# Kernel optimization log

Measured on AMD Instinct MI355X. Metric: run time of the kernel, lower is better.

Reference implementation:

```python
import jax, jax.numpy as jnp
import numpy as np

ORDER = 2
BN_EPS = 1e-5

def setup_inputs() -> dict:
    key = jax.random.key(0)
    ks = jax.random.split(key, 8)
    B, N, L, H = 32, 512, 12, 64
    S = 2                      # support_len
    OUT = 64                   # out_dim
    M = ORDER * S * H          # einsum middle dim = 256
    x = jax.random.normal(ks[0], (B, N, L, H), dtype=jnp.float32)
    # row-scaled random diffusion matrices to keep multi-hop propagation stable
    support = jax.random.uniform(ks[1], (S, N, N), dtype=jnp.float32) / N
    scale = 1.0 / M
    weight = scale * jax.random.normal(ks[2], (L, M, OUT), dtype=jnp.float32)
    eps = jnp.zeros((1,), dtype=jnp.float32)
    gamma = jnp.ones((OUT,), dtype=jnp.float32)
    beta = jnp.zeros((OUT,), dtype=jnp.float32)
    w2 = jax.random.normal(ks[3], (OUT, OUT), dtype=jnp.float32) / np.sqrt(OUT)
    b2 = jnp.zeros((OUT,), dtype=jnp.float32)
    return {"x": x, "support": support, "weight": weight, "eps": eps,
            "gamma": gamma, "beta": beta, "w2": w2, "b2": b2}

def reference(x, support, weight, eps, gamma, beta, w2, b2):
    B, N, L, H = x.shape
    xv = x.reshape(B, N, L * H)            # [B,N,LH]
    res = []
    for i in range(support.shape[0]):      # small fixed loop over supports
        A = support[i]                     # [N,N]
        out = xv
        for _ in range(ORDER):
            out = (1.0 + eps) * out + jnp.einsum('nm,bmd->bnd', A, out)
            res.append(out)
    out = jnp.stack(res, axis=-1)          # [B,N,LH,K], K = order*support_len
    K = out.shape[-1]
    out = out.reshape(B, N, L, H * K)      # [B,N,L,M]
    out = jnp.einsum('bnlm,lmo->bno', out, weight)   # [B,N,OUT]
    # dropout is identity in eval mode
    C = out.shape[-1]
    flat = out.reshape(B * N, C)
    mean = flat.mean(axis=0)
    var = flat.var(axis=0)                 # biased, matching torch BN training
    normed = (flat - mean) * jax.lax.rsqrt(var + BN_EPS) * gamma + beta
    y = jax.nn.relu(normed.reshape(B, N, C))
    return jnp.einsum('bnc,oc->bno', y, w2) + b2
```

## Files before the change

kernel.cpp:

```cpp
#include <hip/hip_runtime.h>
#include <hip/hip_bf16.h>
#include <cstddef>
#include <cstdint>

#define B_   32
#define N_   512
#define D_   768
#define OUT_ 64
#define R_   (B_ * N_)

typedef unsigned short u16;
typedef __bf16 bf16x8 __attribute__((ext_vector_type(8)));
typedef float  f32x4  __attribute__((ext_vector_type(4)));
typedef unsigned short u16x8 __attribute__((ext_vector_type(8)));

__device__ __forceinline__ u16 f2bf(float f) {
    __hip_bfloat16 h = __float2bfloat16(f);
    return __builtin_bit_cast(u16, h);
}

__device__ __forceinline__ f32x4 mfma16(u16x8 a, u16x8 b, f32x4 c) {
    return __builtin_amdgcn_mfma_f32_16x16x32_bf16(
        __builtin_bit_cast(bf16x8, a), __builtin_bit_cast(bf16x8, b), c, 0, 0, 0);
}

__device__ __forceinline__ void gl2lds16(const void* g, void* l) {
    __builtin_amdgcn_global_load_lds(
        (const __attribute__((address_space(1))) unsigned int*)g,
        (__attribute__((address_space(3))) unsigned int*)l, 16, 0, 0);
}

__global__ __launch_bounds__(256) void prep2(
    const float* __restrict__ support, const float* __restrict__ weight,
    const float* __restrict__ epsp,
    u16* __restrict__ MallC, u16* __restrict__ MT, u16* __restrict__ Wt)
{
    const int blk = blockIdx.x, tid = threadIdx.x;
    __shared__ float t[32][33];
    if (blk < 512) {
        int s = blk >> 8, rem = blk & 255;
        int n0 = (rem >> 4) * 32, m0 = (rem & 15) * 32;
        const float f = 1.0f + epsp[0];
        const float* S = support + (size_t)s * 262144;
#pragma unroll
        for (int p = 0; p < 4; ++p) {
            int nl = p * 8 + (tid >> 5), ml = tid & 31;
            float v = S[(size_t)(n0 + nl) * 512 + m0 + ml];
            if (n0 + nl == m0 + ml) v += f;
            MallC[(size_t)(n0 + nl) * 2048 + s * 1024 + m0 + ml] = f2bf(v);
            t[nl][ml] = v;
        }
        __syncthreads();
#pragma unroll
        for (int p = 0; p < 4; ++p) {
            int ml = p * 8 + (tid >> 5), nl = tid & 31;
            MT[(size_t)s * 262144 + (size_t)(m0 + ml) * 512 + n0 + nl] = f2bf(t[nl][ml]);
        }
    } else {
        int idx = (blk - 512) * 256 + tid;
        int k = idx / 49152, rem = idx % 49152;
        int o = rem / 768, d = rem % 768;
        int l = d >> 6, hh = d & 63;
        Wt[idx] = f2bf(weight[((size_t)l * 256 + hh * 4 + k) * 64 + o]);
    }
}

__global__ __launch_bounds__(256) void zgemm_fused(
    const u16* __restrict__ Wt, const float* __restrict__ x,
    const u16* __restrict__ MallC_in, const u16* __restrict__ MT,
    u16* __restrict__ Z, u16* __restrict__ MallC_out)
{
    __shared__ __align__(16) char smem[32768];
    const int tid = threadIdx.x, lane = tid & 63, wid = tid >> 6;
    const int wr = wid >> 1, wc = wid & 1;
    const int lrow = lane & 15, lk = (lane >> 4) * 8;
    const int q = lane >> 4;
    const int bid = blockIdx.x;

    if (bid < 512) {
        u16* As = (u16*)smem;
        u16* Bs = (u16*)(smem + 16384);
        const int rt = bid >> 1, y = bid & 1;
        const int j0 = rt * 64;

        const u16* gsrcA[4]; u16* ldstA[4];
#pragma unroll
        for (int t = 0; t < 4; ++t) {
            int idx = wid * 4 + t;
            int pan = idx >> 3, sub = idx & 7;
            gsrcA[t] = Wt + (size_t)(y * 128 + sub * 16 + lrow) * 768 + pan * 32 + lk;
            ldstA[t] = As + pan * 4096 + sub * 512;
        }
        const int brow = tid & 63, kp = tid >> 6;
        const f32x4* gx = (const f32x4*)(x + (size_t)(j0 + brow) * 768 + kp * 16);
        u16* bdst = Bs + (kp >> 1) * 2048 + (brow >> 4) * 512 + (brow & 15) * 8;
        const int bo0 = (kp & 1) * 2 * 128, bo1 = bo0 + 128;

        f32x4 acc[4][2] = {};
        for (int kk = 0; kk < 12; ++kk) {
#pragma unroll
            for (int t = 0; t < 4; ++t) gl2lds16(gsrcA[t], ldstA[t]);
#pragma unroll
            for (int t = 0; t < 4; ++t) gsrcA[t] += 64;
            f32x4 a0 = gx[0], a1 = gx[1], a2 = gx[2], a3 = gx[3];
            gx += 16;
            u16x8 w0, w1;
#pragma unroll
            for (int j = 0; j < 4; ++j) {
                w0[j] = f2bf(a0[j]); w0[4 + j] = f2bf(a1[j]);
                w1[j] = f2bf(a2[j]); w1[4 + j] = f2bf(a3[j]);
            }
            *(u16x8*)(bdst + bo0) = w0;
            *(u16x8*)(bdst + bo1) = w1;
            __syncthreads();
#pragma unroll
            for (int pan = 0; pan < 2; ++pan) {
                u16x8 af[4], bq[2];
#pragma unroll
                for (int f = 0; f < 4; ++f)
                    af[f] = *(const u16x8*)(As + pan * 4096 + (wr * 4 + f) * 512 + lane * 8);
#pragma unroll
                for (int f = 0; f < 2; ++f)
                    bq[f] = *(const u16x8*)(Bs + pan * 2048 + (wc * 2 + f) * 512 + lane * 8);
#pragma unroll
                for (int fi = 0; fi < 4; ++fi)
#pragma unroll
                    for (int fj = 0; fj < 2; ++fj)
                        acc[fi][fj] = mfma16(af[fi], bq[fj], acc[fi][fj]);
            }
            __syncthreads();
        }
        u16* Rw = (u16*)smem + wid * 2560;
#pragma unroll
        for (int fi = 0; fi < 4; ++fi)
#pragma unroll
            for (int fj = 0; fj < 2; ++fj)
#pragma unroll
                for (int r = 0; r < 4; ++r)
                    Rw[(fi * 16 + q * 4 + r) * 40 + fj * 16 + lrow] = f2bf(acc[fi][fj][r]);
        __syncthreads();
        const int k = y * 2 + wr;
        const int b = rt >> 3;
        const int m0 = (j0 & 511) + wc * 32;
#pragma unroll
        for (int p = 0; p < 4; ++p) {
            int row = p * 16 + (lane >> 2);
            int cc = (lane & 3) * 8;
            u16x8 v = *(const u16x8*)(Rw + row * 40 + cc);
            *(u16x8*)(Z + (size_t)(b * 64 + row) * 2048 + k * 512 + m0 + cc) = v;
        }
    } else {
        u16* St = (u16*)smem;
        int lb = bid - 512;
        int s = lb >> 4, rem = lb & 15;
        int i0 = (rem >> 2) * 128, j0 = (rem & 3) * 128;
        const u16* Ab = MallC_in + s * 1024;
        const u16* Bb = MT + (size_t)s * 262144;

        const u16* gsrc[8]; u16* ldst[8];
#pragma unroll
        for (int t = 0; t < 8; ++t) {
            int idx = wid * 8 + t;
            int pan = idx >> 4, q2 = idx & 15;
            if (q2 < 8) {
                gsrc[t] = Ab + (size_t)(i0 + q2 * 16 + lrow) * 2048 + pan * 32 + lk;
                ldst[t] = St + pan * 8192 + q2 * 512;
            } else {
                gsrc[t] = Bb + (size_t)(j0 + (q2 - 8) * 16 + lrow) * 512 + pan * 32 + lk;
                ldst[t] = St + pan * 8192 + 4096 + (q2 - 8) * 512;
            }
        }
        f32x4 acc[4][4] = {};
        for (int kk = 0; kk < 8; ++kk) {
#pragma unroll
            for (int t = 0; t < 8; ++t) gl2lds16(gsrc[t], ldst[t]);
#pragma unroll
            for (int t = 0; t < 8; ++t) gsrc[t] += 64;
            __syncthreads();
#pragma unroll
            for (int pan = 0; pan < 2; ++pan) {
                u16x8 af[4], bq[4];
#pragma unroll
                for (int f = 0; f < 4; ++f)
                    af[f] = *(const u16x8*)(St + pan * 8192 + (wr * 4 + f) * 512 + lane * 8);
#pragma unroll
                for (int f = 0; f < 4; ++f)
                    bq[f] = *(const u16x8*)(St + pan * 8192 + 4096 + (wc * 4 + f) * 512 + lane * 8);
#pragma unroll
                for (int fi = 0; fi < 4; ++fi)
#pragma unroll
                    for (int fj = 0; fj < 4; ++fj)
                        acc[fi][fj] = mfma16(af[fi], bq[fj], acc[fi][fj]);
            }
            __syncthreads();
        }
#pragma unroll
        for (int fi = 0; fi < 4; ++fi)
#pragma unroll
            for (int fj = 0; fj < 4; ++fj)
#pragma unroll
                for (int r = 0; r < 4; ++r) {
                    int n = i0 + wr * 64 + fi * 16 + q * 4 + r;
                    int c = j0 + wc * 64 + fj * 16 + lrow;
                    MallC_out[(size_t)n * 2048 + (2 * s + 1) * 512 + c] = f2bf(acc[fi][fj][r]);
                }
    }
}

__global__ __launch_bounds__(256) void ysum(
    const u16* __restrict__ MallC, const u16* __restrict__ Z,
    float* __restrict__ Yh)
{
    __shared__ __align__(16) u16 St[8192];
    u16* As = St; u16* Bs = St + 4096;
    const int tid = threadIdx.x, lane = tid & 63, wid = tid >> 6;
    const int wr = wid >> 1, wc = wid & 1;
    const int lrow = lane & 15, lk = (lane >> 4) * 8;
    const int bid = blockIdx.x;
    const int rt = bid & 255, ks = bid >> 8;
    const int r0 = rt * 64, b = rt >> 3, n0 = r0 & 511;
    const size_t km0 = (size_t)ks * 1024;

    const u16* gsrc[4]; u16* ldst[4];
#pragma unroll
    for (int t = 0; t < 4; ++t) {
        int idx = wid * 4 + t;
        int pan = idx >> 3, q2 = idx & 7;
        if (q2 < 4) {
            gsrc[t] = MallC + (size_t)(n0 + q2 * 16 + lrow) * 2048 + km0 + pan * 32 + lk;
            ldst[t] = As + pan * 2048 + q2 * 512;
        } else {
            int s2 = q2 - 4;
            gsrc[t] = Z + (size_t)(b * 64 + s2 * 16 + lrow) * 2048 + km0 + pan * 32 + lk;
            ldst[t] = Bs + pan * 2048 + s2 * 512;
        }
    }
    f32x4 acc[2][2] = {};
    for (int kk = 0; kk < 16; ++kk) {
#pragma unroll
        for (int t = 0; t < 4; ++t) gl2lds16(gsrc[t], ldst[t]);
#pragma unroll
        for (int t = 0; t < 4; ++t) gsrc[t] += 64;
        __syncthreads();
#pragma unroll
        for (int pan = 0; pan < 2; ++pan) {
            u16x8 af[2], bq[2];
#pragma unroll
            for (int f = 0; f < 2; ++f)
                af[f] = *(const u16x8*)(As + pan * 2048 + (wr * 2 + f) * 512 + lane * 8);
#pragma unroll
            for (int f = 0; f < 2; ++f)
                bq[f] = *(const u16x8*)(Bs + pan * 2048 + (wc * 2 + f) * 512 + lane * 8);
#pragma unroll
            for (int fi = 0; fi < 2; ++fi)
#pragma unroll
                for (int fj = 0; fj < 2; ++fj)
                    acc[fi][fj] = mfma16(af[fi], bq[fj], acc[fi][fj]);
        }
        __syncthreads();
    }
    const int q = lane >> 4;
    float* Yk = Yh + (size_t)ks * R_ * 64;
#pragma unroll
    for (int fi = 0; fi < 2; ++fi)
#pragma unroll
        for (int fj = 0; fj < 2; ++fj)
#pragma unroll
            for (int r = 0; r < 4; ++r) {
                int rr = r0 + wr * 32 + fi * 16 + q * 4 + r;
                int o  = wc * 32 + fj * 16 + lrow;
                Yk[(size_t)rr * 64 + o] = acc[fi][fj][r];
            }
}

__global__ __launch_bounds__(256) void bn_part(
    const float* __restrict__ Yh, float* __restrict__ part)
{
    const int blk = blockIdx.x, tid = threadIdx.x;
    const int o = tid & 63, g = tid >> 6;
    float s = 0.f, s2 = 0.f;
#pragma unroll
    for (int p = 0; p < 16; ++p) {
        int r = blk * 64 + p * 4 + g;
        size_t off = (size_t)r * 64 + o;
        float v = Yh[off] + Yh[(size_t)R_ * 64 + off];
        s += v; s2 += v * v;
    }
    __shared__ float ls[4][64], ls2[4][64];
    ls[g][o] = s; ls2[g][o] = s2;
    __syncthreads();
    if (tid < 64) {
        float t = 0.f, t2 = 0.f;
#pragma unroll
        for (int g2 = 0; g2 < 4; ++g2) { t += ls[g2][tid]; t2 += ls2[g2][tid]; }
        part[blk * 128 + tid]      = t;
        part[blk * 128 + 64 + tid] = t2;
    }
}

__global__ __launch_bounds__(256) void bn_final(
    const float* __restrict__ part, const float* __restrict__ gamma,
    const float* __restrict__ beta, float* __restrict__ stats)
{
    const int tid = threadIdx.x;
    const int c = tid & 63, g = tid >> 6;
    float s = 0.f, s2 = 0.f;
    for (int b = g; b < 256; b += 4) {
        s  += part[b * 128 + c];
        s2 += part[b * 128 + 64 + c];
    }
    __shared__ float ls[4][64], ls2[4][64];
    ls[g][c] = s; ls2[g][c] = s2;
    __syncthreads();
    if (tid < 64) {
        float t = 0.f, t2 = 0.f;
#pragma unroll
        for (int g2 = 0; g2 < 4; ++g2) { t += ls[g2][tid]; t2 += ls2[g2][tid]; }
        float mean = t * (1.0f / R_);
        float var  = t2 * (1.0f / R_) - mean * mean;
        float a = rsqrtf(var + 1e-5f) * gamma[tid];
        stats[tid]      = a;
        stats[64 + tid] = beta[tid] - mean * a;
    }
}

__global__ __launch_bounds__(256) void bn_out(
    const float* __restrict__ Yh, const float* __restrict__ stats,
    const float* __restrict__ w2, const float* __restrict__ b2,
    float* __restrict__ out)
{
    __shared__ float ys[64 * 68];
    __shared__ float w2s[64 * 65];
    __shared__ float sa[64], sh[64];
    const int tid = threadIdx.x;
    const int r0 = blockIdx.x * 64;
#pragma unroll
    for (int i = 0; i < 16; ++i) {
        int idx = tid + i * 256;
        w2s[(idx >> 6) * 65 + (idx & 63)] = w2[idx];
    }
    if (tid < 64) { sa[tid] = stats[tid]; sh[tid] = stats[64 + tid]; }
    __syncthreads();
    const int o = tid & 63, g = tid >> 6;
    {
        float a = sa[o], b = sh[o];
#pragma unroll
        for (int p = 0; p < 16; ++p) {
            int rl = p * 4 + g;
            size_t off = (size_t)(r0 + rl) * 64 + o;
            float v = Yh[off] + Yh[(size_t)R_ * 64 + off];
            ys[o * 68 + rl] = fmaxf(fmaf(v, a, b), 0.f);
        }
    }
    __syncthreads();
    float acc[16];
    float bb = b2[o];
#pragma unroll
    for (int j = 0; j < 16; ++j) acc[j] = bb;
    for (int c = 0; c < 64; ++c) {
        float wv = w2s[o * 65 + c];
        const float* yr = ys + c * 68 + g * 16;
        f32x4 y0 = *(const f32x4*)(yr);
        f32x4 y1 = *(const f32x4*)(yr + 4);
        f32x4 y2 = *(const f32x4*)(yr + 8);
        f32x4 y3 = *(const f32x4*)(yr + 12);
#pragma unroll
        for (int j = 0; j < 4; ++j) {
            acc[j]      = fmaf(wv, y0[j], acc[j]);
            acc[4 + j]  = fmaf(wv, y1[j], acc[4 + j]);
            acc[8 + j]  = fmaf(wv, y2[j], acc[8 + j]);
            acc[12 + j] = fmaf(wv, y3[j], acc[12 + j]);
        }
    }
#pragma unroll
    for (int j = 0; j < 16; ++j)
        out[(size_t)(r0 + g * 16 + j) * OUT_ + o] = acc[j];
}

extern "C" void kernel_launch(void* const* d_in, const int* in_sizes, int n_in,
                              void* d_out, int out_size, void* d_ws, size_t ws_size,
                              hipStream_t stream)
{
    const float* x       = (const float*)d_in[0];
    const float* support = (const float*)d_in[1];
    const float* weight  = (const float*)d_in[2];
    const float* eps     = (const float*)d_in[3];
    const float* gamma   = (const float*)d_in[4];
    const float* beta    = (const float*)d_in[5];
    const float* w2      = (const float*)d_in[6];
    const float* b2      = (const float*)d_in[7];
    float* out = (float*)d_out;

    char* ws = (char*)d_ws;
    u16*   MallC = (u16*)(ws);
    u16*   MT    = (u16*)(ws + 2097152);
    u16*   Wt    = (u16*)(ws + 3145728);
    u16*   Z     = (u16*)(ws + 3538944);
    float* Yh    = (float*)(ws + 11927552);
    float* part  = (float*)(ws + 20316160);
    float* stats = (float*)(ws + 20447232);

    prep2     <<<1280, 256, 0, stream>>>(support, weight, eps, MallC, MT, Wt);
    zgemm_fused<<<544, 256, 0, stream>>>(Wt, x, MallC, MT, Z, MallC);
    ysum      <<<512,  256, 0, stream>>>(MallC, Z, Yh);
    bn_part   <<<256,  256, 0, stream>>>(Yh, part);
    bn_final  <<<1,    256, 0, stream>>>(part, gamma, beta, stats);
    bn_out    <<<256,  256, 0, stream>>>(Yh, stats, w2, b2, out);
}
```

Baseline: 172.7 us.

## Retile Z GEMM to full-width weight tiles, prefetch next K-slice, fold BN finalize

```diff
diff --git a/kernel.cpp b/kernel.cpp
--- a/kernel.cpp
+++ b/kernel.cpp
@@ -13,6 +13,11 @@
 typedef __bf16 bf16x8 __attribute__((ext_vector_type(8)));
 typedef float  f32x4  __attribute__((ext_vector_type(4)));
 typedef unsigned short u16x8 __attribute__((ext_vector_type(8)));
+typedef unsigned short u16x4 __attribute__((ext_vector_type(4)));
+
+#define WAITVM(n) __asm__ __volatile__("s_waitcnt vmcnt(" #n ")" ::: "memory")
+#define WAITLGKM() __asm__ __volatile__("s_waitcnt lgkmcnt(0)" ::: "memory")
+#define SBAR()    __builtin_amdgcn_s_barrier()
 
 __device__ __forceinline__ u16 f2bf(float f) {
     __hip_bfloat16 h = __float2bfloat16(f);
@@ -65,93 +70,86 @@
     }
 }
 
-__global__ __launch_bounds__(256) void zgemm_fused(
+__global__ __launch_bounds__(256) void zmsq(
     const u16* __restrict__ Wt, const float* __restrict__ x,
     const u16* __restrict__ MallC_in, const u16* __restrict__ MT,
     u16* __restrict__ Z, u16* __restrict__ MallC_out)
 {
-    __shared__ __align__(16) char smem[32768];
+    __shared__ __align__(16) u16 SM[17408];
     const int tid = threadIdx.x, lane = tid & 63, wid = tid >> 6;
-    const int wr = wid >> 1, wc = wid & 1;
-    const int lrow = lane & 15, lk = (lane >> 4) * 8;
+    const int lrow = lane & 15, lk8 = (lane >> 4) * 8;
     const int q = lane >> 4;
     const int bid = blockIdx.x;
 
-    if (bid < 512) {
-        u16* As = (u16*)smem;
-        u16* Bs = (u16*)(smem + 16384);
-        const int rt = bid >> 1, y = bid & 1;
-        const int j0 = rt * 64;
-
-        const u16* gsrcA[4]; u16* ldstA[4];
-#pragma unroll
-        for (int t = 0; t < 4; ++t) {
-            int idx = wid * 4 + t;
-            int pan = idx >> 3, sub = idx & 7;
-            gsrcA[t] = Wt + (size_t)(y * 128 + sub * 16 + lrow) * 768 + pan * 32 + lk;
-            ldstA[t] = As + pan * 4096 + sub * 512;
-        }
-        const int brow = tid & 63, kp = tid >> 6;
-        const f32x4* gx = (const f32x4*)(x + (size_t)(j0 + brow) * 768 + kp * 16);
-        u16* bdst = Bs + (kp >> 1) * 2048 + (brow >> 4) * 512 + (brow & 15) * 8;
-        const int bo0 = (kp & 1) * 2 * 128, bo1 = bo0 + 128;
-
-        f32x4 acc[4][2] = {};
+    if (bid < 1024) {
+        const int mt = bid;
+        const int b = mt >> 5, mm0 = (mt & 31) * 16;
+
+        const u16* gsrcA[8]; u16* ldstA[8];
+#pragma unroll
+        for (int t = 0; t < 8; ++t) {
+            int idx = wid * 8 + t;
+            int pan = idx >> 4, sub = idx & 15;
+            gsrcA[t] = Wt + (size_t)(sub * 16 + lrow) * 768 + pan * 32 + lk8;
+            ldstA[t] = SM + pan * 8192 + sub * 512;
+        }
+        const int r = tid >> 4, kc = tid & 15;
+        const float* gx = x + (size_t)(mt * 16 + r) * 768 + kc * 4;
+        const int kin = kc * 4;
+        const int pan = kin >> 5, kp = kin & 31;
+        u16* bdst = SM + 16384 + pan * 512 + (kp >> 3) * 128 + r * 8 + (kp & 7);
+
+        f32x4 bv = *(const f32x4*)(gx);
+#pragma unroll
+        for (int t = 0; t < 8; ++t) gl2lds16(gsrcA[t], ldstA[t]);
+        WAITVM(8);
+        { u16x4 w; for (int j = 0; j < 4; ++j) w[j] = f2bf(bv[j]); *(u16x4*)bdst = w; }
+        WAITVM(0); WAITLGKM();
+        SBAR();
+
+        f32x4 acc[4] = {};
+        u16x8 Af[4][2], Bf[2];
+#pragma unroll
         for (int kk = 0; kk < 12; ++kk) {
 #pragma unroll
-            for (int t = 0; t < 4; ++t) gl2lds16(gsrcA[t], ldstA[t]);
-#pragma unroll
-            for (int t = 0; t < 4; ++t) gsrcA[t] += 64;
-            f32x4 a0 = gx[0], a1 = gx[1], a2 = gx[2], a3 = gx[3];
-            gx += 16;
-            u16x8 w0, w1;
-#pragma unroll
-            for (int j = 0; j < 4; ++j) {
-                w0[j] = f2bf(a0[j]); w0[4 + j] = f2bf(a1[j]);
-                w1[j] = f2bf(a2[j]); w1[4 + j] = f2bf(a3[j]);
-            }
-            *(u16x8*)(bdst + bo0) = w0;
-            *(u16x8*)(bdst + bo1) = w1;
-            __syncthreads();
-#pragma unroll
-            for (int pan = 0; pan < 2; ++pan) {
-                u16x8 af[4], bq[2];
-#pragma unroll
-                for (int f = 0; f < 4; ++f)
-                    af[f] = *(const u16x8*)(As + pan * 4096 + (wr * 4 + f) * 512 + lane * 8);
-#pragma unroll
-                for (int f = 0; f < 2; ++f)
-                    bq[f] = *(const u16x8*)(Bs + pan * 2048 + (wc * 2 + f) * 512 + lane * 8);
+            for (int fi = 0; fi < 4; ++fi)
+#pragma unroll
+                for (int p2 = 0; p2 < 2; ++p2)
+                    Af[fi][p2] = *(const u16x8*)(SM + p2 * 8192 + (wid * 4 + fi) * 512 + lane * 8);
+#pragma unroll
+            for (int p2 = 0; p2 < 2; ++p2)
+                Bf[p2] = *(const u16x8*)(SM + 16384 + p2 * 512 + lane * 8);
+            WAITLGKM();
+            SBAR();
+            if (kk < 11) {
+                bv = *(const f32x4*)(gx + (kk + 1) * 64);
+#pragma unroll
+                for (int t = 0; t < 8; ++t) {
+                    gl2lds16(gsrcA[t] + (kk + 1) * 64, ldstA[t]);
+                }
+            }
+#pragma unroll
+            for (int p2 = 0; p2 < 2; ++p2)
 #pragma unroll
                 for (int fi = 0; fi < 4; ++fi)
-#pragma unroll
-                    for (int fj = 0; fj < 2; ++fj)
-                        acc[fi][fj] = mfma16(af[fi], bq[fj], acc[fi][fj]);
-            }
-            __syncthreads();
-        }
-        u16* Rw = (u16*)smem + wid * 2560;
+                    acc[fi] = mfma16(Af[fi][p2], Bf[p2], acc[fi]);
+            if (kk < 11) {
+                WAITVM(8);
+                { u16x4 w; for (int j = 0; j < 4; ++j) w[j] = f2bf(bv[j]); *(u16x4*)bdst = w; }
+                WAITVM(0); WAITLGKM();
+                SBAR();
+            }
+        }
 #pragma unroll
         for (int fi = 0; fi < 4; ++fi)
 #pragma unroll
-            for (int fj = 0; fj < 2; ++fj)
-#pragma unroll
-                for (int r = 0; r < 4; ++r)
-                    Rw[(fi * 16 + q * 4 + r) * 40 + fj * 16 + lrow] = f2bf(acc[fi][fj][r]);
-        __syncthreads();
-        const int k = y * 2 + wr;
-        const int b = rt >> 3;
-        const int m0 = (j0 & 511) + wc * 32;
-#pragma unroll
-        for (int p = 0; p < 4; ++p) {
-            int row = p * 16 + (lane >> 2);
-            int cc = (lane & 3) * 8;
-            u16x8 v = *(const u16x8*)(Rw + row * 40 + cc);
-            *(u16x8*)(Z + (size_t)(b * 64 + row) * 2048 + k * 512 + m0 + cc) = v;
-        }
+            for (int rr = 0; rr < 4; ++rr) {
+                int o = fi * 16 + q * 4 + rr;
+                Z[(size_t)(b * 64 + o) * 2048 + wid * 512 + mm0 + lrow] = f2bf(acc[fi][rr]);
+            }
     } else {
-        u16* St = (u16*)smem;
-        int lb = bid - 512;
+        const int wr = wid >> 1, wc = wid & 1;
+        int lb = bid - 1024;
         int s = lb >> 4, rem = lb & 15;
         int i0 = (rem >> 2) * 128, j0 = (rem & 3) * 128;
         const u16* Ab = MallC_in + s * 1024;
@@ -163,11 +161,11 @@
             int idx = wid * 8 + t;
             int pan = idx >> 4, q2 = idx & 15;
             if (q2 < 8) {
-                gsrc[t] = Ab + (size_t)(i0 + q2 * 16 + lrow) * 2048 + pan * 32 + lk;
-                ldst[t] = St + pan * 8192 + q2 * 512;
+                gsrc[t] = Ab + (size_t)(i0 + q2 * 16 + lrow) * 2048 + pan * 32 + lk8;
+                ldst[t] = SM + pan * 8192 + q2 * 512;
             } else {
-                gsrc[t] = Bb + (size_t)(j0 + (q2 - 8) * 16 + lrow) * 512 + pan * 32 + lk;
-                ldst[t] = St + pan * 8192 + 4096 + (q2 - 8) * 512;
+                gsrc[t] = Bb + (size_t)(j0 + (q2 - 8) * 16 + lrow) * 512 + pan * 32 + lk8;
+                ldst[t] = SM + pan * 8192 + 4096 + (q2 - 8) * 512;
             }
         }
         f32x4 acc[4][4] = {};
@@ -182,10 +180,10 @@
                 u16x8 af[4], bq[4];
 #pragma unroll
                 for (int f = 0; f < 4; ++f)
-                    af[f] = *(const u16x8*)(St + pan * 8192 + (wr * 4 + f) * 512 + lane * 8);
+                    af[f] = *(const u16x8*)(SM + pan * 8192 + (wr * 4 + f) * 512 + lane * 8);
 #pragma unroll
                 for (int f = 0; f < 4; ++f)
-                    bq[f] = *(const u16x8*)(St + pan * 8192 + 4096 + (wc * 4 + f) * 512 + lane * 8);
+                    bq[f] = *(const u16x8*)(SM + pan * 8192 + 4096 + (wc * 4 + f) * 512 + lane * 8);
 #pragma unroll
                 for (int fi = 0; fi < 4; ++fi)
 #pragma unroll
@@ -199,23 +197,21 @@
 #pragma unroll
             for (int fj = 0; fj < 4; ++fj)
 #pragma unroll
-                for (int r = 0; r < 4; ++r) {
-                    int n = i0 + wr * 64 + fi * 16 + q * 4 + r;
+                for (int rr = 0; rr < 4; ++rr) {
+                    int n = i0 + wr * 64 + fi * 16 + q * 4 + rr;
                     int c = j0 + wc * 64 + fj * 16 + lrow;
-                    MallC_out[(size_t)n * 2048 + (2 * s + 1) * 512 + c] = f2bf(acc[fi][fj][r]);
+                    MallC_out[(size_t)n * 2048 + (2 * s + 1) * 512 + c] = f2bf(acc[fi][fj][rr]);
                 }
     }
 }
 
 __global__ __launch_bounds__(256) void ysum(
-    const u16* __restrict__ MallC, const u16* __restrict__ Z,
-    float* __restrict__ Yh)
-{
-    __shared__ __align__(16) u16 St[8192];
-    u16* As = St; u16* Bs = St + 4096;
+    const u16* __restrict__ G, const u16* __restrict__ Z, float* __restrict__ Yh)
+{
+    __shared__ __align__(16) u16 SM[8192];
     const int tid = threadIdx.x, lane = tid & 63, wid = tid >> 6;
     const int wr = wid >> 1, wc = wid & 1;
-    const int lrow = lane & 15, lk = (lane >> 4) * 8;
+    const int lrow = lane & 15, lk8 = (lane >> 4) * 8;
     const int bid = blockIdx.x;
     const int rt = bid & 255, ks = bid >> 8;
     const int r0 = rt * 64, b = rt >> 3, n0 = r0 & 511;
@@ -225,39 +221,51 @@
 #pragma unroll
     for (int t = 0; t < 4; ++t) {
         int idx = wid * 4 + t;
-        int pan = idx >> 3, q2 = idx & 7;
-        if (q2 < 4) {
-            gsrc[t] = MallC + (size_t)(n0 + q2 * 16 + lrow) * 2048 + km0 + pan * 32 + lk;
-            ldst[t] = As + pan * 2048 + q2 * 512;
+        if (idx < 8) {
+            int pan = idx >> 2, sub = idx & 3;
+            gsrc[t] = G + (size_t)(n0 + sub * 16 + lrow) * 2048 + km0 + pan * 32 + lk8;
+            ldst[t] = SM + pan * 2048 + sub * 512;
         } else {
-            int s2 = q2 - 4;
-            gsrc[t] = Z + (size_t)(b * 64 + s2 * 16 + lrow) * 2048 + km0 + pan * 32 + lk;
-            ldst[t] = Bs + pan * 2048 + s2 * 512;
-        }
-    }
+            int i2 = idx - 8;
+            int pan = i2 >> 2, sub = i2 & 3;
+            gsrc[t] = Z + (size_t)(b * 64 + sub * 16 + lrow) * 2048 + km0 + pan * 32 + lk8;
+            ldst[t] = SM + 4096 + pan * 2048 + sub * 512;
+        }
+    }
+#pragma unroll
+    for (int t = 0; t < 4; ++t) gl2lds16(gsrc[t], ldst[t]);
+    WAITVM(0);
+    SBAR();
+
     f32x4 acc[2][2] = {};
+    u16x8 Af[2][2], Bfr[2][2];
+#pragma unroll
     for (int kk = 0; kk < 16; ++kk) {
 #pragma unroll
-        for (int t = 0; t < 4; ++t) gl2lds16(gsrc[t], ldst[t]);
-#pragma unroll
-        for (int t = 0; t < 4; ++t) gsrc[t] += 64;
-        __syncthreads();
-#pragma unroll
-        for (int pan = 0; pan < 2; ++pan) {
-            u16x8 af[2], bq[2];
-#pragma unroll
-            for (int f = 0; f < 2; ++f)
-                af[f] = *(const u16x8*)(As + pan * 2048 + (wr * 2 + f) * 512 + lane * 8);
-#pragma unroll
-            for (int f = 0; f < 2; ++f)
-                bq[f] = *(const u16x8*)(Bs + pan * 2048 + (wc * 2 + f) * 512 + lane * 8);
+        for (int p2 = 0; p2 < 2; ++p2) {
+#pragma unroll
+            for (int f = 0; f < 2; ++f) {
+                Af[f][p2]  = *(const u16x8*)(SM + p2 * 2048 + (wr * 2 + f) * 512 + lane * 8);
+                Bfr[f][p2] = *(const u16x8*)(SM + 4096 + p2 * 2048 + (wc * 2 + f) * 512 + lane * 8);
+            }
+        }
+        WAITLGKM();
+        SBAR();
+        if (kk < 15) {
+#pragma unroll
+            for (int t = 0; t < 4; ++t) gl2lds16(gsrc[t] + (kk + 1) * 64, ldst[t]);
+        }
+#pragma unroll
+        for (int p2 = 0; p2 < 2; ++p2)
 #pragma unroll
             for (int fi = 0; fi < 2; ++fi)
 #pragma unroll
                 for (int fj = 0; fj < 2; ++fj)
-                    acc[fi][fj] = mfma16(af[fi], bq[fj], acc[fi][fj]);
-        }
-        __syncthreads();
+                    acc[fi][fj] = mfma16(Af[fi][p2], Bfr[fj][p2], acc[fi][fj]);
+        if (kk < 15) {
+            WAITVM(0);
+            SBAR();
+        }
     }
     const int q = lane >> 4;
     float* Yk = Yh + (size_t)ks * R_ * 64;
@@ -266,10 +274,10 @@
 #pragma unroll
         for (int fj = 0; fj < 2; ++fj)
 #pragma unroll
-            for (int r = 0; r < 4; ++r) {
-                int rr = r0 + wr * 32 + fi * 16 + q * 4 + r;
+            for (int rr = 0; rr < 4; ++rr) {
+                int r2 = r0 + wr * 32 + fi * 16 + q * 4 + rr;
                 int o  = wc * 32 + fj * 16 + lrow;
-                Yk[(size_t)rr * 64 + o] = acc[fi][fj][r];
+                Yk[(size_t)r2 * 64 + o] = acc[fi][fj][rr];
             }
 }
 
@@ -298,58 +306,51 @@
     }
 }
 
-__global__ __launch_bounds__(256) void bn_final(
-    const float* __restrict__ part, const float* __restrict__ gamma,
-    const float* __restrict__ beta, float* __restrict__ stats)
-{
-    const int tid = threadIdx.x;
-    const int c = tid & 63, g = tid >> 6;
-    float s = 0.f, s2 = 0.f;
-    for (int b = g; b < 256; b += 4) {
-        s  += part[b * 128 + c];
-        s2 += part[b * 128 + 64 + c];
-    }
-    __shared__ float ls[4][64], ls2[4][64];
-    ls[g][c] = s; ls2[g][c] = s2;
-    __syncthreads();
-    if (tid < 64) {
-        float t = 0.f, t2 = 0.f;
-#pragma unroll
-        for (int g2 = 0; g2 < 4; ++g2) { t += ls[g2][tid]; t2 += ls2[g2][tid]; }
-        float mean = t * (1.0f / R_);
-        float var  = t2 * (1.0f / R_) - mean * mean;
-        float a = rsqrtf(var + 1e-5f) * gamma[tid];
-        stats[tid]      = a;
-        stats[64 + tid] = beta[tid] - mean * a;
-    }
-}
-
 __global__ __launch_bounds__(256) void bn_out(
-    const float* __restrict__ Yh, const float* __restrict__ stats,
+    const float* __restrict__ Yh, const float* __restrict__ part,
+    const float* __restrict__ gamma, const float* __restrict__ beta,
     const float* __restrict__ w2, const float* __restrict__ b2,
     float* __restrict__ out)
 {
     __shared__ float ys[64 * 68];
     __shared__ float w2s[64 * 65];
+    __shared__ float red[4][64], red2[4][64];
     __shared__ float sa[64], sh[64];
     const int tid = threadIdx.x;
     const int r0 = blockIdx.x * 64;
+    const int o = tid & 63, g = tid >> 6;
+    {
+        float s = 0.f, s2 = 0.f;
+        for (int p = g; p < 256; p += 4) {
+            s  += part[p * 128 + o];
+            s2 += part[p * 128 + 64 + o];
+        }
+        red[g][o] = s; red2[g][o] = s2;
+    }
 #pragma unroll
     for (int i = 0; i < 16; ++i) {
         int idx = tid + i * 256;
         w2s[(idx >> 6) * 65 + (idx & 63)] = w2[idx];
     }
-    if (tid < 64) { sa[tid] = stats[tid]; sh[tid] = stats[64 + tid]; }
     __syncthreads();
-    const int o = tid & 63, g = tid >> 6;
+    if (tid < 64) {
+        float t0 = red[0][tid] + red[1][tid] + red[2][tid] + red[3][tid];
+        float t2 = red2[0][tid] + red2[1][tid] + red2[2][tid] + red2[3][tid];
+        float mean = t0 * (1.0f / R_);
+        float var  = t2 * (1.0f / R_) - mean * mean;
+        float a = rsqrtf(var + 1e-5f) * gamma[tid];
+        sa[tid] = a;
+        sh[tid] = beta[tid] - mean * a;
+    }
+    __syncthreads();
     {
-        float a = sa[o], b = sh[o];
+        float a = sa[o], bsh = sh[o];
 #pragma unroll
         for (int p = 0; p < 16; ++p) {
             int rl = p * 4 + g;
             size_t off = (size_t)(r0 + rl) * 64 + o;
             float v = Yh[off] + Yh[(size_t)R_ * 64 + off];
-            ys[o * 68 + rl] = fmaxf(fmaf(v, a, b), 0.f);
+            ys[o * 68 + rl] = fmaxf(fmaf(v, a, bsh), 0.f);
         }
     }
     __syncthreads();
@@ -398,12 +399,10 @@
     u16*   Z     = (u16*)(ws + 3538944);
     float* Yh    = (float*)(ws + 11927552);
     float* part  = (float*)(ws + 20316160);
-    float* stats = (float*)(ws + 20447232);
-
-    prep2     <<<1280, 256, 0, stream>>>(support, weight, eps, MallC, MT, Wt);
-    zgemm_fused<<<544, 256, 0, stream>>>(Wt, x, MallC, MT, Z, MallC);
-    ysum      <<<512,  256, 0, stream>>>(MallC, Z, Yh);
-    bn_part   <<<256,  256, 0, stream>>>(Yh, part);
-    bn_final  <<<1,    256, 0, stream>>>(part, gamma, beta, stats);
-    bn_out    <<<256,  256, 0, stream>>>(Yh, stats, w2, b2, out);
-}
+
+    prep2  <<<1280, 256, 0, stream>>>(support, weight, eps, MallC, MT, Wt);
+    zmsq   <<<1056, 256, 0, stream>>>(Wt, x, MallC, MT, Z, MallC);
+    ysum   <<<512,  256, 0, stream>>>(MallC, Z, Yh);
+    bn_part<<<256,  256, 0, stream>>>(Yh, part);
+    bn_out <<<256,  256, 0, stream>>>(Yh, part, gamma, beta, w2, b2, out);
+}
```

Result: slower. 212.6 us (+23.0%).
